# Optimization experiments

Hardware: AMD Instinct MI355X
Metric: run time of the kernel (lower is better)

Reference implementation:

```python
import jax, jax.numpy as jnp
import numpy as np

DIM_IN, DIM_Q, DIM_K, DIM_S, DIM_MLP_S, L, B = 512, 128, 128, 256, 128, 512, 32


def setup_inputs() -> dict:
    key = jax.random.key(0)
    ks = jax.random.split(key, 16)
    s = lambda fan_in: 1.0 / np.sqrt(fan_in)
    inp = {
        "query": jax.random.normal(ks[0], (B, L, DIM_IN), jnp.float32),
        "key": jax.random.normal(ks[1], (B, L, DIM_IN), jnp.float32),
        "value": jax.random.normal(ks[2], (B, L, DIM_IN), jnp.float32),
        "sf": jax.random.normal(ks[3], (B, DIM_S), jnp.float32),
        "atten_mask": jax.random.randint(ks[4], (B, L, L), 0, 2).astype(bool),
        # linear weights stored (in, out); y = x @ W + b
        "Wq": jax.random.normal(ks[5], (DIM_IN, DIM_Q), jnp.float32) * s(DIM_IN),
        "bq": jnp.zeros((DIM_Q,), jnp.float32),
        "Wk": jax.random.normal(ks[6], (DIM_IN, DIM_K), jnp.float32) * s(DIM_IN),
        "bk": jnp.zeros((DIM_K,), jnp.float32),
        "Wv": jax.random.normal(ks[7], (DIM_IN, DIM_K), jnp.float32) * s(DIM_IN),
        "bv": jnp.zeros((DIM_K,), jnp.float32),
        "Wb1": jax.random.normal(ks[8], (DIM_S, DIM_MLP_S), jnp.float32) * s(DIM_S),
        "bb1": jnp.zeros((DIM_MLP_S,), jnp.float32),
        "Wb2": jax.random.normal(ks[9], (DIM_MLP_S, L * L), jnp.float32) * s(DIM_MLP_S),
        "bb2": jnp.zeros((L * L,), jnp.float32),
    }
    return inp


def reference(query, key, value, sf, atten_mask, Wq, bq, Wk, bk, Wv, bv, Wb1, bb1, Wb2, bb2):
    b, l, d = query.shape
    q = query @ Wq + bq          # [b, l, dim_q]
    k = key @ Wk + bk            # [b, l, dim_k]
    v = value @ Wv + bv          # [b, l, dim_k]
    # bias MLP: Linear -> ReLU -> Linear, reshaped to [b, l, l]
    bias = (jax.nn.relu(sf @ Wb1 + bb1) @ Wb2 + bb2).reshape(b, l, l)
    scale = q.shape[-1] ** 0.5
    scores = jnp.einsum("bld,bmd->blm", q, k) / scale
    # faithful to masked_fill_(mask, 1e-9): masked positions become 1e-9, NOT -inf
    scores = jnp.where(atten_mask, jnp.asarray(1e-9, scores.dtype), scores)
    attn = jax.nn.softmax(scores, axis=-1) + bias   # bias added AFTER softmax
    out = jnp.einsum("blm,bmd->bld", attn, v)
    return out
```

## Files before the change

### kernel.cpp

```cpp
#include <hip/hip_runtime.h>


typedef unsigned int   u32;
typedef unsigned short u16;
typedef __attribute__((ext_vector_type(8))) short bf16x8;
typedef __attribute__((ext_vector_type(4))) float f32x4;
typedef __attribute__((ext_vector_type(4))) u32   u32x4;

__device__ __forceinline__ float B2F(u16 x) { return __uint_as_float(((u32)x) << 16); }
__device__ __forceinline__ u16 f2bf(float f) {
    u32 u = __float_as_uint(f);
    return (u16)((u + 0x7fffu + ((u >> 16) & 1u)) >> 16);
}

__global__ __launch_bounds__(256) void mask_detect(const u32* __restrict__ m,
                                                   u32* __restrict__ flag)
{
    const size_t t = (size_t)blockIdx.x * 256 + threadIdx.x;
    u32 any = 0;
#pragma unroll
    for (int l = 0; l < 4; ++l) any |= (m[t * 4 + l] > 1u) ? 1u : 0u;
    if (__ballot(any)) {
        if ((threadIdx.x & 63) == 0) atomicOr(flag, 1u);
    }
}

__global__ __launch_bounds__(256) void mask_canon(const void* __restrict__ mask,
                                                  const u32* __restrict__ flag,
                                                  unsigned char* __restrict__ canon)
{
    const size_t i = (size_t)blockIdx.x * 256 + threadIdx.x;
    if (*flag == 0) canon[i] = (((const int*)mask)[i] != 0) ? 1 : 0;
    else            canon[i] = (((const unsigned char*)mask)[i] != 0) ? 1 : 0;
}

__global__ __launch_bounds__(256) void wtrans(
    const float* __restrict__ Wq, const float* __restrict__ Wk, const float* __restrict__ Wv,
    u16* __restrict__ WT)
{
    const float* W = (blockIdx.y == 0) ? Wq : (blockIdx.y == 1) ? Wk : Wv;
    __shared__ u16 Ts[64][136];
    const int tid = threadIdx.x, kt = blockIdx.x;

    {
        const int kk = tid >> 2, nseg = tid & 3;
        const float4* src = (const float4*)(W + (size_t)(kt * 64 + kk) * 128 + nseg * 32);
#pragma unroll
        for (int j = 0; j < 8; ++j) {
            float4 v = src[j];
            Ts[kk][nseg * 32 + j * 4 + 0] = f2bf(v.x);
            Ts[kk][nseg * 32 + j * 4 + 1] = f2bf(v.y);
            Ts[kk][nseg * 32 + j * 4 + 2] = f2bf(v.z);
            Ts[kk][nseg * 32 + j * 4 + 3] = f2bf(v.w);
        }
    }
    __syncthreads();
    {
        const int n = tid >> 1, kseg = tid & 1;
        u32 pk[16];
#pragma unroll
        for (int j = 0; j < 16; ++j)
            pk[j] = (u32)Ts[kseg * 32 + 2 * j][n] | ((u32)Ts[kseg * 32 + 2 * j + 1][n] << 16);
        u32x4* dst = (u32x4*)(WT + (size_t)blockIdx.y * 65536 + (size_t)n * 512 + kt * 64 + kseg * 32);
        dst[0] = (u32x4){pk[0], pk[1], pk[2], pk[3]};
        dst[1] = (u32x4){pk[4], pk[5], pk[6], pk[7]};
        dst[2] = (u32x4){pk[8], pk[9], pk[10], pk[11]};
        dst[3] = (u32x4){pk[12], pk[13], pk[14], pk[15]};
    }
}

__global__ __launch_bounds__(256) void proj_mfma(
    const float* __restrict__ Xq, const float* __restrict__ Xk, const float* __restrict__ Xv,
    const u16* __restrict__ WT,
    const float* __restrict__ Bq, const float* __restrict__ Bk, const float* __restrict__ Bv,
    u16* __restrict__ Yq, u16* __restrict__ Yk, u16* __restrict__ YvT)
{
    const int s = blockIdx.y;
    const float* X; const float* Bi;
    if (s == 0)      { X = Xq; Bi = Bq; }
    else if (s == 1) { X = Xk; Bi = Bk; }
    else             { X = Xv; Bi = Bv; }
    const u16* Wn = WT + (size_t)s * 65536;

    __shared__ u16 Xs[64][72];
    __shared__ u16 Ws[128][72];

    const int tid  = threadIdx.x;
    const int w    = tid >> 6;
    const int lane = tid & 63;
    const int c    = lane & 15;
    const int qd   = lane >> 4;
    const int R0   = blockIdx.x * 64;

    f32x4 acc[8];
#pragma unroll
    for (int t = 0; t < 8; ++t) acc[t] = (f32x4){0.f, 0.f, 0.f, 0.f};

    for (int kc = 0; kc < 8; ++kc) {
        __syncthreads();
        {
            const int row = tid >> 2, seg = tid & 3;
            const float4* src = (const float4*)(X + (size_t)(R0 + row) * 512 + kc * 64 + seg * 16);
            float4 v0 = src[0], v1 = src[1], v2 = src[2], v3 = src[3];
            u32 pk[8];
            pk[0] = (u32)f2bf(v0.x) | ((u32)f2bf(v0.y) << 16);
            pk[1] = (u32)f2bf(v0.z) | ((u32)f2bf(v0.w) << 16);
            pk[2] = (u32)f2bf(v1.x) | ((u32)f2bf(v1.y) << 16);
            pk[3] = (u32)f2bf(v1.z) | ((u32)f2bf(v1.w) << 16);
            pk[4] = (u32)f2bf(v2.x) | ((u32)f2bf(v2.y) << 16);
            pk[5] = (u32)f2bf(v2.z) | ((u32)f2bf(v2.w) << 16);
            pk[6] = (u32)f2bf(v3.x) | ((u32)f2bf(v3.y) << 16);
            pk[7] = (u32)f2bf(v3.z) | ((u32)f2bf(v3.w) << 16);
            u32x4* dst = (u32x4*)&Xs[row][seg * 16];
            dst[0] = (u32x4){pk[0], pk[1], pk[2], pk[3]};
            dst[1] = (u32x4){pk[4], pk[5], pk[6], pk[7]};
        }
        {
            const int n = tid >> 1, seg = tid & 1;
            const u32x4* src = (const u32x4*)(Wn + (size_t)n * 512 + kc * 64 + seg * 32);
            u32x4 v0 = src[0], v1 = src[1], v2 = src[2], v3 = src[3];
            u32x4* dst = (u32x4*)&Ws[n][seg * 32];
            dst[0] = v0; dst[1] = v1; dst[2] = v2; dst[3] = v3;
        }
        __syncthreads();

#pragma unroll
        for (int ks = 0; ks < 2; ++ks) {
            if (s < 2) {
                const bf16x8 a = *(const bf16x8*)&Xs[w * 16 + c][ks * 32 + qd * 8];
#pragma unroll
                for (int nt = 0; nt < 8; ++nt) {
                    const bf16x8 b = *(const bf16x8*)&Ws[nt * 16 + c][ks * 32 + qd * 8];
                    acc[nt] = __builtin_amdgcn_mfma_f32_16x16x32_bf16(a, b, acc[nt], 0, 0, 0);
                }
            } else {
#pragma unroll
                for (int t = 0; t < 2; ++t) {
                    const bf16x8 a = *(const bf16x8*)&Ws[(2 * w + t) * 16 + c][ks * 32 + qd * 8];
#pragma unroll
                    for (int it = 0; it < 4; ++it) {
                        const bf16x8 b = *(const bf16x8*)&Xs[it * 16 + c][ks * 32 + qd * 8];
                        acc[t * 4 + it] = __builtin_amdgcn_mfma_f32_16x16x32_bf16(a, b, acc[t * 4 + it], 0, 0, 0);
                    }
                }
            }
        }
    }

    if (s < 2) {
        u16* Y = (s == 0) ? Yq : Yk;
#pragma unroll
        for (int nt = 0; nt < 8; ++nt) {
            const float bn = Bi[nt * 16 + c];
#pragma unroll
            for (int r = 0; r < 4; ++r)
                Y[(size_t)(R0 + w * 16 + qd * 4 + r) * 128 + nt * 16 + c] = f2bf(acc[nt][r] + bn);
        }
    } else {
        const int bb = blockIdx.x >> 3, il0 = R0 & 511;
#pragma unroll
        for (int t = 0; t < 2; ++t)
#pragma unroll
            for (int r = 0; r < 4; ++r) {
                const int d = (2 * w + t) * 16 + qd * 4 + r;
                const float bd = Bi[d];
#pragma unroll
                for (int it = 0; it < 4; ++it)
                    YvT[(size_t)bb * 65536 + (size_t)d * 512 + il0 + it * 16 + c] =
                        f2bf(acc[t * 4 + it][r] + bd);
            }
    }
}

__global__ __launch_bounds__(256) void mlp1_kernel(
    const float* __restrict__ sf, const float* __restrict__ Wb1,
    const float* __restrict__ bb1, float* __restrict__ h)
{
    const int t = blockIdx.x * 256 + threadIdx.x;
    const int b = t >> 7, n = t & 127;
    float acc = bb1[n];
    for (int m = 0; m < 256; ++m)
        acc += sf[b * 256 + m] * Wb1[m * 128 + n];
    h[t] = fmaxf(acc, 0.0f);
}

__global__ __launch_bounds__(256) void bias_mlp2(
    const float* __restrict__ h, const float* __restrict__ Wb2,
    const float* __restrict__ bb2, u16* __restrict__ biasb)
{
    __shared__ float hs[4096];
    const int tid = threadIdx.x;
#pragma unroll
    for (int l = 0; l < 16; ++l) hs[l * 256 + tid] = h[l * 256 + tid];
    __syncthreads();

    const size_t n = (size_t)blockIdx.x * 256 + tid;
    float acc[32];
    const float bb = bb2[n];
#pragma unroll
    for (int b = 0; b < 32; ++b) acc[b] = bb;

    for (int m4 = 0; m4 < 32; ++m4) {
        const float w0 = Wb2[(size_t)(m4 * 4 + 0) * 262144 + n];
        const float w1 = Wb2[(size_t)(m4 * 4 + 1) * 262144 + n];
        const float w2 = Wb2[(size_t)(m4 * 4 + 2) * 262144 + n];
        const float w3 = Wb2[(size_t)(m4 * 4 + 3) * 262144 + n];
#pragma unroll
        for (int b = 0; b < 32; ++b) {
            const float4 hv = *(const float4*)&hs[b * 128 + m4 * 4];
            acc[b] += hv.x * w0 + hv.y * w1 + hv.z * w2 + hv.w * w3;
        }
    }
#pragma unroll
    for (int b = 0; b < 32; ++b)
        biasb[(size_t)b * 262144 + n] = f2bf(acc[b]);
}

__global__ __launch_bounds__(256, 1) void attn_mfma(
    const u16* __restrict__ qb, const u16* __restrict__ kb, const u16* __restrict__ vTb,
    const unsigned char* __restrict__ canon, const u16* __restrict__ biasb,
    float* __restrict__ out)
{
    __shared__ u16 Qs[64 * 136];
    __shared__ u16 Ks[64 * 136];
    __shared__ u16 Ps[64 * 72];
    __shared__ u16 Vs[128 * 72];

    const int tid  = threadIdx.x;
    const int w    = tid >> 6;
    const int lane = tid & 63;
    const int c    = lane & 15;
    const int qd   = lane >> 4;
    const int bb   = blockIdx.x >> 3;
    const int it   = blockIdx.x & 7;
    const int i0   = it * 64;

    {
        const int r = tid >> 2, sg = tid & 3;
        const u32x4* src = (const u32x4*)(qb + ((size_t)bb * 512 + i0 + r) * 128 + sg * 32);
        u32x4 v0 = src[0], v1 = src[1], v2 = src[2], v3 = src[3];
        u32x4* dst = (u32x4*)&Qs[r * 136 + sg * 32];
        dst[0] = v0; dst[1] = v1; dst[2] = v2; dst[3] = v3;
    }

    f32x4 S[8][4];
#pragma unroll
    for (int jt = 0; jt < 8; ++jt)
#pragma unroll
        for (int jj = 0; jj < 4; ++jj) S[jt][jj] = (f32x4){0.f, 0.f, 0.f, 0.f};

    for (int jt = 0; jt < 8; ++jt) {
        __syncthreads();
        {
            const int r = tid >> 2, sg = tid & 3;
            const u32x4* src = (const u32x4*)(kb + ((size_t)bb * 512 + jt * 64 + r) * 128 + sg * 32);
            u32x4 v0 = src[0], v1 = src[1], v2 = src[2], v3 = src[3];
            u32x4* dst = (u32x4*)&Ks[r * 136 + sg * 32];
            dst[0] = v0; dst[1] = v1; dst[2] = v2; dst[3] = v3;
        }
        __syncthreads();
#pragma unroll
        for (int kc = 0; kc < 4; ++kc) {
            const bf16x8 a = *(const bf16x8*)&Qs[(w * 16 + c) * 136 + kc * 32 + qd * 8];
#pragma unroll
            for (int jj = 0; jj < 4; ++jj) {
                const bf16x8 b = *(const bf16x8*)&Ks[(jj * 16 + c) * 136 + kc * 32 + qd * 8];
                S[jt][jj] = __builtin_amdgcn_mfma_f32_16x16x32_bf16(a, b, S[jt][jj], 0, 0, 0);
            }
        }
    }

    const float sc = 0.08838834764831845f;
    float inv[4];
#pragma unroll
    for (int r = 0; r < 4; ++r) {
        const unsigned char* mp = canon + ((size_t)bb * 512 + i0 + w * 16 + qd * 4 + r) * 512;
        float mx = -3.4e38f;
#pragma unroll
        for (int jt = 0; jt < 8; ++jt)
#pragma unroll
            for (int jj = 0; jj < 4; ++jj) {
                float s = S[jt][jj][r] * sc;
                if (mp[jt * 64 + jj * 16 + c]) s = 1e-9f;
                S[jt][jj][r] = s;
                mx = fmaxf(mx, s);
            }
#pragma unroll
        for (int o = 1; o < 16; o <<= 1) mx = fmaxf(mx, __shfl_xor(mx, o, 64));
        float sm = 0.f;
#pragma unroll
        for (int jt = 0; jt < 8; ++jt)
#pragma unroll
            for (int jj = 0; jj < 4; ++jj) {
                const float e = __expf(S[jt][jj][r] - mx);
                S[jt][jj][r] = e;
                sm += e;
            }
#pragma unroll
        for (int o = 1; o < 16; o <<= 1) sm += __shfl_xor(sm, o, 64);
        inv[r] = 1.0f / sm;
    }

    f32x4 O[8];
#pragma unroll
    for (int ns = 0; ns < 8; ++ns) O[ns] = (f32x4){0.f, 0.f, 0.f, 0.f};

    for (int jt = 0; jt < 8; ++jt) {
        __syncthreads();
#pragma unroll
        for (int r = 0; r < 4; ++r) {
            const u16* bp = biasb + (size_t)bb * 262144
                          + ((size_t)i0 + w * 16 + qd * 4 + r) * 512 + jt * 64;
#pragma unroll
            for (int jj = 0; jj < 4; ++jj) {
                const float p = S[jt][jj][r] * inv[r] + B2F(bp[jj * 16 + c]);
                Ps[(w * 16 + qd * 4 + r) * 72 + jj * 16 + c] = f2bf(p);
            }
        }
        {
            const int d = tid >> 1, sg = tid & 1;
            const u32x4* src = (const u32x4*)(vTb + (size_t)bb * 65536 + (size_t)d * 512
                                              + jt * 64 + sg * 32);
            u32x4 v0 = src[0], v1 = src[1], v2 = src[2], v3 = src[3];
            u32x4* dst = (u32x4*)&Vs[d * 72 + sg * 32];
            dst[0] = v0; dst[1] = v1; dst[2] = v2; dst[3] = v3;
        }
        __syncthreads();
#pragma unroll
        for (int kc = 0; kc < 2; ++kc) {
            const bf16x8 a = *(const bf16x8*)&Ps[(w * 16 + c) * 72 + kc * 32 + qd * 8];
#pragma unroll
            for (int ns = 0; ns < 8; ++ns) {
                const bf16x8 b = *(const bf16x8*)&Vs[(ns * 16 + c) * 72 + kc * 32 + qd * 8];
                O[ns] = __builtin_amdgcn_mfma_f32_16x16x32_bf16(a, b, O[ns], 0, 0, 0);
            }
        }
    }

#pragma unroll
    for (int ns = 0; ns < 8; ++ns)
#pragma unroll
        for (int r = 0; r < 4; ++r)
            out[((size_t)bb * 512 + i0 + w * 16 + qd * 4 + r) * 128 + ns * 16 + c] = O[ns][r];
}

extern "C" void kernel_launch(void* const* d_in, const int* in_sizes, int n_in,
                              void* d_out, int out_size, void* d_ws, size_t ws_size,
                              hipStream_t stream)
{
    const float* query = (const float*)d_in[0];
    const float* key_  = (const float*)d_in[1];
    const float* value = (const float*)d_in[2];
    const float* sf    = (const float*)d_in[3];
    const void*  mask  = d_in[4];
    const float* Wq  = (const float*)d_in[5];
    const float* bq  = (const float*)d_in[6];
    const float* Wk  = (const float*)d_in[7];
    const float* bk  = (const float*)d_in[8];
    const float* Wv  = (const float*)d_in[9];
    const float* bv  = (const float*)d_in[10];
    const float* Wb1 = (const float*)d_in[11];
    const float* bb1 = (const float*)d_in[12];
    const float* Wb2 = (const float*)d_in[13];
    const float* bb2 = (const float*)d_in[14];
    float* out = (float*)d_out;

    char* w = (char*)d_ws;
    u32*   flag  = (u32*)(w);
    unsigned char* canon = (unsigned char*)(w + (1u << 20));
    u16*   qb    = (u16*)(w + (16u << 20));
    u16*   kb    = (u16*)(w + (24u << 20));
    u16*   vTb   = (u16*)(w + (32u << 20));
    float* h     = (float*)(w + (40u << 20));
    u16*   biasb = (u16*)(w + (41u << 20));
    u16*   WT    = (u16*)(w + (58u << 20));

    hipMemsetAsync(flag, 0, 4, stream);
    mask_detect<<<2048, 256, 0, stream>>>((const u32*)mask, flag);
    mask_canon<<<32768, 256, 0, stream>>>(mask, flag, canon);
    wtrans<<<dim3(8, 3), 256, 0, stream>>>(Wq, Wk, Wv, WT);
    proj_mfma<<<dim3(256, 3), 256, 0, stream>>>(query, key_, value, WT,
                                                bq, bk, bv, qb, kb, vTb);
    mlp1_kernel<<<16, 256, 0, stream>>>(sf, Wb1, bb1, h);
    bias_mlp2<<<1024, 256, 0, stream>>>(h, Wb2, bb2, biasb);
    attn_mfma<<<256, 256, 0, stream>>>(qb, kb, vTb, canon, biasb, out);
}
```

Baseline: 383.4 us.

## Split attention key range across two warp groups and skip mask canonicalization

The attention kernel now runs 512 threads per block. Two 256-thread groups each handle half of the key columns, combine their row max and row sum through shared memory, and add their partial outputs at the end. K, V and bias tiles are prefetched into registers and double buffered so global loads overlap MFMA work, and the block order is changed. The host also chooses the mask path from the input byte sizes: a byte-sized mask is used directly and an int32 mask gets a single conversion kernel, which drops the detect and canon launches. The aim is more waves per CU and fewer preprocessing passes, at the cost of extra synchronisation and reliance on size-based dtype inference.

```diff
diff --git a/kernel.cpp b/kernel.cpp
--- a/kernel.cpp
+++ b/kernel.cpp
@@ -32,6 +32,13 @@
     const size_t i = (size_t)blockIdx.x * 256 + threadIdx.x;
     if (*flag == 0) canon[i] = (((const int*)mask)[i] != 0) ? 1 : 0;
     else            canon[i] = (((const unsigned char*)mask)[i] != 0) ? 1 : 0;
+}
+
+__global__ __launch_bounds__(256) void mask_canon_i32(const int* __restrict__ m,
+                                                      unsigned char* __restrict__ canon)
+{
+    const size_t i = (size_t)blockIdx.x * 256 + threadIdx.x;
+    canon[i] = (m[i] != 0) ? 1 : 0;
 }
 
 __global__ __launch_bounds__(256) void wtrans(
@@ -216,132 +223,209 @@
         biasb[(size_t)b * 262144 + n] = f2bf(acc[b]);
 }
 
-__global__ __launch_bounds__(256, 1) void attn_mfma(
+__global__ __launch_bounds__(512, 2) void attn_mfma8(
     const u16* __restrict__ qb, const u16* __restrict__ kb, const u16* __restrict__ vTb,
     const unsigned char* __restrict__ canon, const u16* __restrict__ biasb,
     float* __restrict__ out)
 {
-    __shared__ u16 Qs[64 * 136];
-    __shared__ u16 Ks[64 * 136];
-    __shared__ u16 Ps[64 * 72];
-    __shared__ u16 Vs[128 * 72];
+    __shared__ alignas(16) u16 Ks[2][64 * 136];
+    __shared__ alignas(16) u16 Ps[2][64 * 72];
+    __shared__ alignas(16) u16 Vs[2][128 * 72];
+    __shared__ alignas(16) u16 Bs[2][64 * 72];
+    __shared__ float redm[2][64];
+    __shared__ float reds[2][64];
 
     const int tid  = threadIdx.x;
-    const int w    = tid >> 6;
+    const int g    = tid >> 8;
+    const int gtid = tid & 255;
+    const int wl   = (tid >> 6) & 3;
     const int lane = tid & 63;
     const int c    = lane & 15;
     const int qd   = lane >> 4;
-    const int bb   = blockIdx.x >> 3;
-    const int it   = blockIdx.x & 7;
+    const int bb   = blockIdx.x & 31;
+    const int it   = blockIdx.x >> 5;
     const int i0   = it * 64;
 
-    {
-        const int r = tid >> 2, sg = tid & 3;
-        const u32x4* src = (const u32x4*)(qb + ((size_t)bb * 512 + i0 + r) * 128 + sg * 32);
-        u32x4 v0 = src[0], v1 = src[1], v2 = src[2], v3 = src[3];
-        u32x4* dst = (u32x4*)&Qs[r * 136 + sg * 32];
-        dst[0] = v0; dst[1] = v1; dst[2] = v2; dst[3] = v3;
-    }
-
-    f32x4 S[8][4];
-#pragma unroll
-    for (int jt = 0; jt < 8; ++jt)
+    bf16x8 qf[4];
+    {
+        const u16* qp = qb + ((size_t)bb * 512 + i0 + wl * 16 + c) * 128 + qd * 8;
+#pragma unroll
+        for (int kc = 0; kc < 4; ++kc) qf[kc] = *(const bf16x8*)(qp + kc * 32);
+    }
+
+    const int kr_ = gtid >> 2, ksg = gtid & 3;
+    const u16* kbase = kb + ((size_t)bb * 512 + g * 256) * 128;
+    {
+        const u32x4* src = (const u32x4*)(kbase + (size_t)kr_ * 128 + ksg * 32);
+        u32x4 k0 = src[0], k1 = src[1], k2 = src[2], k3 = src[3];
+        u32x4* dst = (u32x4*)&Ks[g][kr_ * 136 + ksg * 32];
+        dst[0] = k0; dst[1] = k1; dst[2] = k2; dst[3] = k3;
+    }
+    __syncthreads();
+
+    f32x4 S[4][4];
+#pragma unroll
+    for (int jt = 0; jt < 4; ++jt)
 #pragma unroll
         for (int jj = 0; jj < 4; ++jj) S[jt][jj] = (f32x4){0.f, 0.f, 0.f, 0.f};
 
-    for (int jt = 0; jt < 8; ++jt) {
+#pragma unroll
+    for (int jt = 0; jt < 4; ++jt) {
+        u32x4 k0, k1, k2, k3;
+        if (jt < 3) {
+            const u32x4* src = (const u32x4*)(kbase + ((size_t)(jt + 1) * 64 + kr_) * 128 + ksg * 32);
+            k0 = src[0]; k1 = src[1]; k2 = src[2]; k3 = src[3];
+        }
+#pragma unroll
+        for (int kc = 0; kc < 4; ++kc) {
+            const bf16x8 a = qf[kc];
+#pragma unroll
+            for (int jj = 0; jj < 4; ++jj) {
+                const bf16x8 b = *(const bf16x8*)&Ks[g][(jj * 16 + c) * 136 + kc * 32 + qd * 8];
+                S[jt][jj] = __builtin_amdgcn_mfma_f32_16x16x32_bf16(a, b, S[jt][jj], 0, 0, 0);
+            }
+        }
+        if (jt < 3) {
+            __syncthreads();
+            u32x4* dst = (u32x4*)&Ks[g][kr_ * 136 + ksg * 32];
+            dst[0] = k0; dst[1] = k1; dst[2] = k2; dst[3] = k3;
+            __syncthreads();
+        }
+    }
+
+    const int vd = gtid >> 1, vsg = gtid & 1;
+    const int brw = gtid >> 2, bsg = gtid & 3;
+    const u16* vbase = vTb + (size_t)bb * 65536;
+    const u16* bbase = biasb + (size_t)bb * 262144;
+    u32x4 vr0, vr1, vr2, vr3, br0, br1;
+    {
+        const u32x4* sv = (const u32x4*)(vbase + (size_t)vd * 512 + (g * 4) * 64 + vsg * 32);
+        vr0 = sv[0]; vr1 = sv[1]; vr2 = sv[2]; vr3 = sv[3];
+        const u32x4* sb = (const u32x4*)(bbase + (size_t)(i0 + brw) * 512 + (g * 4) * 64 + bsg * 16);
+        br0 = sb[0]; br1 = sb[1];
+    }
+
+    const float sc = 0.08838834764831845f;
+    float lm[4];
+#pragma unroll
+    for (int r = 0; r < 4; ++r) {
+        const int lrow = wl * 16 + qd * 4 + r;
+        const unsigned char* cp = canon + ((size_t)bb * 512 + i0 + lrow) * 512 + g * 256;
+        float mx = -3.4e38f;
+#pragma unroll
+        for (int jt = 0; jt < 4; ++jt)
+#pragma unroll
+            for (int jj = 0; jj < 4; ++jj) {
+                float s = S[jt][jj][r] * sc;
+                if (cp[jt * 64 + jj * 16 + c]) s = 1e-9f;
+                S[jt][jj][r] = s;
+                mx = fmaxf(mx, s);
+            }
+#pragma unroll
+        for (int o = 1; o < 16; o <<= 1) mx = fmaxf(mx, __shfl_xor(mx, o, 64));
+        lm[r] = mx;
+    }
+    if (c == 0) {
+#pragma unroll
+        for (int r = 0; r < 4; ++r) redm[g][wl * 16 + qd * 4 + r] = lm[r];
+    }
+    __syncthreads();
+    float ls[4];
+#pragma unroll
+    for (int r = 0; r < 4; ++r) {
+        const int lrow = wl * 16 + qd * 4 + r;
+        const float gmx = fmaxf(redm[0][lrow], redm[1][lrow]);
+        float sm = 0.f;
+#pragma unroll
+        for (int jt = 0; jt < 4; ++jt)
+#pragma unroll
+            for (int jj = 0; jj < 4; ++jj) {
+                const float e = __expf(S[jt][jj][r] - gmx);
+                S[jt][jj][r] = e;
+                sm += e;
+            }
+#pragma unroll
+        for (int o = 1; o < 16; o <<= 1) sm += __shfl_xor(sm, o, 64);
+        ls[r] = sm;
+    }
+    if (c == 0) {
+#pragma unroll
+        for (int r = 0; r < 4; ++r) reds[g][wl * 16 + qd * 4 + r] = ls[r];
+    }
+    __syncthreads();
+    float inv_[4];
+#pragma unroll
+    for (int r = 0; r < 4; ++r) {
+        const int lrow = wl * 16 + qd * 4 + r;
+        inv_[r] = 1.0f / (reds[0][lrow] + reds[1][lrow]);
+    }
+
+    f32x4 O_[8];
+#pragma unroll
+    for (int ns = 0; ns < 8; ++ns) O_[ns] = (f32x4){0.f, 0.f, 0.f, 0.f};
+
+#pragma unroll
+    for (int jt = 0; jt < 4; ++jt) {
         __syncthreads();
         {
-            const int r = tid >> 2, sg = tid & 3;
-            const u32x4* src = (const u32x4*)(kb + ((size_t)bb * 512 + jt * 64 + r) * 128 + sg * 32);
-            u32x4 v0 = src[0], v1 = src[1], v2 = src[2], v3 = src[3];
-            u32x4* dst = (u32x4*)&Ks[r * 136 + sg * 32];
-            dst[0] = v0; dst[1] = v1; dst[2] = v2; dst[3] = v3;
+            u32x4* dv = (u32x4*)&Vs[g][vd * 72 + vsg * 32];
+            dv[0] = vr0; dv[1] = vr1; dv[2] = vr2; dv[3] = vr3;
+            u32x4* db = (u32x4*)&Bs[g][brw * 72 + bsg * 16];
+            db[0] = br0; db[1] = br1;
         }
         __syncthreads();
-#pragma unroll
-        for (int kc = 0; kc < 4; ++kc) {
-            const bf16x8 a = *(const bf16x8*)&Qs[(w * 16 + c) * 136 + kc * 32 + qd * 8];
+        if (jt < 3) {
+            const int tg = g * 4 + jt + 1;
+            const u32x4* sv = (const u32x4*)(vbase + (size_t)vd * 512 + tg * 64 + vsg * 32);
+            vr0 = sv[0]; vr1 = sv[1]; vr2 = sv[2]; vr3 = sv[3];
+            const u32x4* sb = (const u32x4*)(bbase + (size_t)(i0 + brw) * 512 + tg * 64 + bsg * 16);
+            br0 = sb[0]; br1 = sb[1];
+        }
+#pragma unroll
+        for (int r = 0; r < 4; ++r) {
+            const int lrow = wl * 16 + qd * 4 + r;
 #pragma unroll
             for (int jj = 0; jj < 4; ++jj) {
-                const bf16x8 b = *(const bf16x8*)&Ks[(jj * 16 + c) * 136 + kc * 32 + qd * 8];
-                S[jt][jj] = __builtin_amdgcn_mfma_f32_16x16x32_bf16(a, b, S[jt][jj], 0, 0, 0);
-            }
-        }
-    }
-
-    const float sc = 0.08838834764831845f;
-    float inv[4];
-#pragma unroll
-    for (int r = 0; r < 4; ++r) {
-        const unsigned char* mp = canon + ((size_t)bb * 512 + i0 + w * 16 + qd * 4 + r) * 512;
-        float mx = -3.4e38f;
-#pragma unroll
-        for (int jt = 0; jt < 8; ++jt)
-#pragma unroll
-            for (int jj = 0; jj < 4; ++jj) {
-                float s = S[jt][jj][r] * sc;
-                if (mp[jt * 64 + jj * 16 + c]) s = 1e-9f;
-                S[jt][jj][r] = s;
-                mx = fmaxf(mx, s);
-            }
-#pragma unroll
-        for (int o = 1; o < 16; o <<= 1) mx = fmaxf(mx, __shfl_xor(mx, o, 64));
-        float sm = 0.f;
-#pragma unroll
-        for (int jt = 0; jt < 8; ++jt)
-#pragma unroll
-            for (int jj = 0; jj < 4; ++jj) {
-                const float e = __expf(S[jt][jj][r] - mx);
-                S[jt][jj][r] = e;
-                sm += e;
-            }
-#pragma unroll
-        for (int o = 1; o < 16; o <<= 1) sm += __shfl_xor(sm, o, 64);
-        inv[r] = 1.0f / sm;
-    }
-
-    f32x4 O[8];
-#pragma unroll
-    for (int ns = 0; ns < 8; ++ns) O[ns] = (f32x4){0.f, 0.f, 0.f, 0.f};
-
-    for (int jt = 0; jt < 8; ++jt) {
+                const float p = S[jt][jj][r] * inv_[r] + B2F(Bs[g][lrow * 72 + jj * 16 + c]);
+                Ps[g][lrow * 72 + jj * 16 + c] = f2bf(p);
+            }
+        }
         __syncthreads();
 #pragma unroll
-        for (int r = 0; r < 4; ++r) {
-            const u16* bp = biasb + (size_t)bb * 262144
-                          + ((size_t)i0 + w * 16 + qd * 4 + r) * 512 + jt * 64;
-#pragma unroll
-            for (int jj = 0; jj < 4; ++jj) {
-                const float p = S[jt][jj][r] * inv[r] + B2F(bp[jj * 16 + c]);
-                Ps[(w * 16 + qd * 4 + r) * 72 + jj * 16 + c] = f2bf(p);
-            }
-        }
-        {
-            const int d = tid >> 1, sg = tid & 1;
-            const u32x4* src = (const u32x4*)(vTb + (size_t)bb * 65536 + (size_t)d * 512
-                                              + jt * 64 + sg * 32);
-            u32x4 v0 = src[0], v1 = src[1], v2 = src[2], v3 = src[3];
-            u32x4* dst = (u32x4*)&Vs[d * 72 + sg * 32];
-            dst[0] = v0; dst[1] = v1; dst[2] = v2; dst[3] = v3;
-        }
-        __syncthreads();
-#pragma unroll
         for (int kc = 0; kc < 2; ++kc) {
-            const bf16x8 a = *(const bf16x8*)&Ps[(w * 16 + c) * 72 + kc * 32 + qd * 8];
+            const bf16x8 a = *(const bf16x8*)&Ps[g][(wl * 16 + c) * 72 + kc * 32 + qd * 8];
 #pragma unroll
             for (int ns = 0; ns < 8; ++ns) {
-                const bf16x8 b = *(const bf16x8*)&Vs[(ns * 16 + c) * 72 + kc * 32 + qd * 8];
-                O[ns] = __builtin_amdgcn_mfma_f32_16x16x32_bf16(a, b, O[ns], 0, 0, 0);
-            }
-        }
-    }
-
-#pragma unroll
-    for (int ns = 0; ns < 8; ++ns)
-#pragma unroll
-        for (int r = 0; r < 4; ++r)
-            out[((size_t)bb * 512 + i0 + w * 16 + qd * 4 + r) * 128 + ns * 16 + c] = O[ns][r];
+                const bf16x8 b = *(const bf16x8*)&Vs[g][(ns * 16 + c) * 72 + kc * 32 + qd * 8];
+                O_[ns] = __builtin_amdgcn_mfma_f32_16x16x32_bf16(a, b, O_[ns], 0, 0, 0);
+            }
+        }
+    }
+
+    __syncthreads();
+    float* Oc = (float*)&Ks[0][0];
+    if (g == 1) {
+#pragma unroll
+        for (int ns = 0; ns < 8; ++ns)
+#pragma unroll
+            for (int r = 0; r < 4; ++r)
+                Oc[(wl * 16 + qd * 4 + r) * 128 + ns * 16 + c] = O_[ns][r];
+    }
+    __syncthreads();
+    if (g == 0) {
+#pragma unroll
+        for (int ns = 0; ns < 8; ++ns)
+#pragma unroll
+            for (int r = 0; r < 4; ++r)
+                Oc[(wl * 16 + qd * 4 + r) * 128 + ns * 16 + c] += O_[ns][r];
+    }
+    __syncthreads();
+    {
+        const int row = tid >> 3, sg = tid & 7;
+        const float4* s4 = (const float4*)&Oc[row * 128 + sg * 16];
+        float4* d4 = (float4*)(out + ((size_t)bb * 512 + i0 + row) * 128 + sg * 16);
+        d4[0] = s4[0]; d4[1] = s4[1]; d4[2] = s4[2]; d4[3] = s4[3];
+    }
 }
 
 extern "C" void kernel_launch(void* const* d_in, const int* in_sizes, int n_in,
@@ -366,8 +450,8 @@
     float* out = (float*)d_out;
 
     char* w = (char*)d_ws;
-    u32*   flag  = (u32*)(w);
-    unsigned char* canon = (unsigned char*)(w + (1u << 20));
+    u32*   flag     = (u32*)(w);
+    unsigned char* canonbuf = (unsigned char*)(w + (1u << 20));
     u16*   qb    = (u16*)(w + (16u << 20));
     u16*   kb    = (u16*)(w + (24u << 20));
     u16*   vTb   = (u16*)(w + (32u << 20));
@@ -375,13 +459,24 @@
     u16*   biasb = (u16*)(w + (41u << 20));
     u16*   WT    = (u16*)(w + (58u << 20));
 
-    hipMemsetAsync(flag, 0, 4, stream);
-    mask_detect<<<2048, 256, 0, stream>>>((const u32*)mask, flag);
-    mask_canon<<<32768, 256, 0, stream>>>(mask, flag, canon);
+    const unsigned char* canon;
+    const bool bytes_conv = (n_in >= 15 && in_sizes[0] == 33554432);
+    if (bytes_conv && in_sizes[4] == 8388608) {
+        canon = (const unsigned char*)mask;
+    } else if (bytes_conv && in_sizes[4] == 33554432) {
+        mask_canon_i32<<<32768, 256, 0, stream>>>((const int*)mask, canonbuf);
+        canon = canonbuf;
+    } else {
+        hipMemsetAsync(flag, 0, 4, stream);
+        mask_detect<<<2048, 256, 0, stream>>>((const u32*)mask, flag);
+        mask_canon<<<32768, 256, 0, stream>>>(mask, flag, canonbuf);
+        canon = canonbuf;
+    }
+
     wtrans<<<dim3(8, 3), 256, 0, stream>>>(Wq, Wk, Wv, WT);
     proj_mfma<<<dim3(256, 3), 256, 0, stream>>>(query, key_, value, WT,
                                                 bq, bk, bv, qb, kb, vTb);
     mlp1_kernel<<<16, 256, 0, stream>>>(sf, Wb1, bb1, h);
     bias_mlp2<<<1024, 256, 0, stream>>>(h, Wb2, bb2, biasb);
-    attn_mfma<<<256, 256, 0, stream>>>(qb, kb, vTb, canon, biasb, out);
-}
+    attn_mfma8<<<256, 512, 0, stream>>>(qb, kb, vTb, canon, biasb, out);
+}
```

Result: no change. 378.1 us (-1.4%).
